# Kernel optimization log

Hardware: AMD Instinct MI355X
Metric: run time of the kernel (lower is better)

## Reference

```python
import jax, jax.numpy as jnp
import numpy as np

EPS = 1e-8  # torch F.cosine_similarity norm clamp


def setup_inputs() -> dict:
    key = jax.random.key(0)
    kq, km = jax.random.split(key)
    b, c, h, w = 4, 128, 16, 16
    n_mem = 2000
    query_feature = jax.random.normal(kq, (b, c, h, w), dtype=jnp.float32)
    memory_bank = jax.random.normal(km, (n_mem, b, c, h, w), dtype=jnp.float32)
    return {"query_feature": query_feature, "memory_bank": memory_bank, "k": 20}


def reference(query_feature, memory_bank, k):
    b = query_feature.shape[0]
    n = memory_bank.shape[0]
    # Flatten per-batch features: query [b, D], memory [N, b, D]
    qf = query_feature.reshape(b, -1)
    mf = memory_bank.reshape(n, b, -1)
    # Cosine similarity along feature dim (torch clamps each norm by eps)
    qn = qf / jnp.maximum(jnp.linalg.norm(qf, axis=-1, keepdims=True), EPS)
    mn = mf / jnp.maximum(jnp.linalg.norm(mf, axis=-1, keepdims=True), EPS)
    sims = jnp.einsum('bd,nbd->n', qn, mn) / b  # mean over batch -> [N]
    top_vals, top_idx = jax.lax.top_k(sims, k)
    weights = jax.nn.softmax(top_vals)  # [k]
    # Weighted gather-sum of selected memory items -> [b, c, h, w]
    selected = memory_bank[top_idx]  # [k, b, c, h, w]
    weighted_sum = jnp.einsum('k,kbchw->bchw', weights, selected)
    return weighted_sum
```

## Files before the change

kernel.cpp:

```cpp
#include <hip/hip_runtime.h>
#include <hip/hip_bf16.h>
#include <math.h>

#define BQ    4
#define DIM   32768
#define DIM4  8192
#define ITEM4 32768
#define EPS   1e-8f
#define QREG  16

__global__ __launch_bounds__(512) void dot_norm_kernel(
        const float* __restrict__ q, const float* __restrict__ mem,
        float2* __restrict__ dn, int N) {
    const int b    = blockIdx.x & 3;
    const int bn   = blockIdx.x >> 2;
    const int nblk = gridDim.x >> 2;
    const int wid  = threadIdx.x >> 6;
    const int lane = threadIdx.x & 63;

    const float4* q4 = (const float4*)(q + (size_t)b * DIM);
    float4 qr[QREG];
    #pragma unroll
    for (int j = 0; j < QREG; ++j) qr[j] = q4[threadIdx.x + j * 512];

    __shared__ float sd[2][8], sn[2][8];
    int buf = 0;

    for (int n = bn; n < N; n += nblk, buf ^= 1) {
        const float4* m4 = (const float4*)(mem + ((size_t)n * BQ + b) * DIM);
        float dot = 0.f, nrm = 0.f;
        #pragma unroll
        for (int j = 0; j < QREG; ++j) {
            float4 m = m4[threadIdx.x + j * 512];
            float4 a = qr[j];
            dot += a.x * m.x + a.y * m.y + a.z * m.z + a.w * m.w;
            nrm += m.x * m.x + m.y * m.y + m.z * m.z + m.w * m.w;
        }
        #pragma unroll
        for (int off = 32; off > 0; off >>= 1) {
            dot += __shfl_down(dot, off);
            nrm += __shfl_down(nrm, off);
        }
        if (lane == 0) { sd[buf][wid] = dot; sn[buf][wid] = nrm; }
        __syncthreads();
        if (threadIdx.x == 0) {
            float d = 0.f, n2 = 0.f;
            #pragma unroll
            for (int w = 0; w < 8; ++w) { d += sd[buf][w]; n2 += sn[buf][w]; }
            dn[n * BQ + b] = make_float2(d, n2);
        }
    }
}

__global__ __launch_bounds__(512) void topk_softmax_kernel(
        const float* __restrict__ q,
        const float2* __restrict__ dn,
        const int* __restrict__ kp,
        float* __restrict__ weights,
        int* __restrict__ topidx,
        int N) {
    const int k    = *kp;
    const int lane = threadIdx.x & 63;
    const int wid  = threadIdx.x >> 6;

    __shared__ float sq[8];
    __shared__ float qden[BQ];
    __shared__ float swv[8];
    __shared__ int   swi[8];
    __shared__ int   sbi;
    __shared__ float tvals[64];
    __shared__ int   tidxs[64];

    {
        const int b = wid & 3, half = wid >> 2;
        const float4* q4 = (const float4*)(q + (size_t)b * DIM) + half * (DIM4 / 2);
        float s = 0.f;
        #pragma unroll 8
        for (int j = 0; j < 64; ++j) {
            float4 v = q4[lane + j * 64];
            s += v.x * v.x + v.y * v.y + v.z * v.z + v.w * v.w;
        }
        #pragma unroll
        for (int off = 32; off > 0; off >>= 1) s += __shfl_down(s, off);
        if (lane == 0) sq[wid] = s;
    }
    __syncthreads();
    if (threadIdx.x < BQ)
        qden[threadIdx.x] = fmaxf(sqrtf(sq[threadIdx.x] + sq[threadIdx.x + 4]), EPS);
    __syncthreads();

    float sv[4];
    #pragma unroll
    for (int i = 0; i < 4; ++i) {
        const int n = threadIdx.x + i * 512;
        if (n < N) {
            const float4* p4 = (const float4*)(dn + (size_t)n * BQ);
            float4 v0 = p4[0];
            float4 v1 = p4[1];
            float s = v0.x / (qden[0] * fmaxf(sqrtf(v0.y), EPS))
                    + v0.z / (qden[1] * fmaxf(sqrtf(v0.w), EPS))
                    + v1.x / (qden[2] * fmaxf(sqrtf(v1.y), EPS))
                    + v1.z / (qden[3] * fmaxf(sqrtf(v1.w), EPS));
            sv[i] = s * (1.0f / BQ);
        } else {
            sv[i] = -INFINITY;
        }
    }

    for (int it = 0; it < k; ++it) {
        float best = sv[0];
        int bi = threadIdx.x;
        #pragma unroll
        for (int i = 1; i < 4; ++i) {
            if (sv[i] > best) { best = sv[i]; bi = threadIdx.x + i * 512; }
        }
        #pragma unroll
        for (int off = 32; off > 0; off >>= 1) {
            float ov = __shfl_down(best, off);
            int   oi = __shfl_down(bi, off);
            if (ov > best || (ov == best && oi < bi)) { best = ov; bi = oi; }
        }
        if (lane == 0) { swv[wid] = best; swi[wid] = bi; }
        __syncthreads();
        if (threadIdx.x == 0) {
            float bv = swv[0]; int bx = swi[0];
            #pragma unroll
            for (int w = 1; w < 8; ++w) {
                if (swv[w] > bv || (swv[w] == bv && swi[w] < bx)) { bv = swv[w]; bx = swi[w]; }
            }
            tvals[it] = bv;
            tidxs[it] = bx;
            sbi = bx;
        }
        __syncthreads();
        const int won = sbi;
        if ((won & 511) == (int)threadIdx.x) sv[won >> 9] = -INFINITY;
    }

    if (threadIdx.x == 0) {
        float m = tvals[0];
        float sum = 0.f;
        for (int i = 0; i < k; ++i) sum += expf(tvals[i] - m);
        float inv = 1.0f / sum;
        for (int i = 0; i < k; ++i) {
            weights[i] = expf(tvals[i] - m) * inv;
            topidx[i]  = tidxs[i];
        }
    }
}

__global__ __launch_bounds__(256) void wsum_kernel(
        const float* __restrict__ mem,
        const float* __restrict__ weights,
        const int* __restrict__ topidx,
        const int* __restrict__ kp,
        float* __restrict__ out) {
    const int k = *kp;
    __shared__ float w[64];
    __shared__ int   id[64];
    if ((int)threadIdx.x < k) {
        w[threadIdx.x]  = weights[threadIdx.x];
        id[threadIdx.x] = topidx[threadIdx.x];
    }
    __syncthreads();
    const int t = blockIdx.x * blockDim.x + threadIdx.x;
    if (t >= ITEM4) return;
    const float4* m4 = (const float4*)mem;
    float4 acc = {0.f, 0.f, 0.f, 0.f};
    for (int j = 0; j < k; ++j) {
        float4 v = m4[(size_t)id[j] * ITEM4 + t];
        float wj = w[j];
        acc.x += wj * v.x; acc.y += wj * v.y; acc.z += wj * v.z; acc.w += wj * v.w;
    }
    ((float4*)out)[t] = acc;
}

extern "C" void kernel_launch(void* const* d_in, const int* in_sizes, int n_in,
                              void* d_out, int out_size, void* d_ws, size_t ws_size,
                              hipStream_t stream) {
    const float* q   = (const float*)d_in[0];
    const float* mem = (const float*)d_in[1];
    const int*   kp  = (const int*)d_in[2];
    float* out = (float*)d_out;

    const int N = in_sizes[1] / (BQ * DIM);

    float2* dn   = (float2*)d_ws;
    float*  wts  = (float*)(dn + (size_t)N * BQ);
    int*    tidx = (int*)(wts + 64);

    dot_norm_kernel<<<2048, 512, 0, stream>>>(q, mem, dn, N);
    topk_softmax_kernel<<<1, 512, 0, stream>>>(q, dn, kp, wts, tidx, N);
    wsum_kernel<<<(ITEM4 + 255) / 256, 256, 0, stream>>>(mem, wts, tidx, kp, out);
}
```

Measured before the change: 217.2 us.

## Use nontemporal streaming loads, single-barrier top-k, and smaller wsum blocks

The memory bank scan in dot_norm now uses nontemporal vector loads so streamed data does not pollute the cache. The top-k loop uses double-buffered shared slots, letting every thread reduce the wave winners itself and dropping one barrier per iteration. The weighted-sum kernel drops to 128-thread blocks and unrolls its gather loop to put more loads in flight. The nontemporal hint may also evict lines that the later gather could have reused.

```diff
diff --git a/kernel.cpp b/kernel.cpp
--- a/kernel.cpp
+++ b/kernel.cpp
@@ -9,6 +9,8 @@
 #define EPS   1e-8f
 #define QREG  16
 
+using f4 = __attribute__((ext_vector_type(4))) float;
+
 __global__ __launch_bounds__(512) void dot_norm_kernel(
         const float* __restrict__ q, const float* __restrict__ mem,
         float2* __restrict__ dn, int N) {
@@ -18,8 +20,8 @@
     const int wid  = threadIdx.x >> 6;
     const int lane = threadIdx.x & 63;
 
-    const float4* q4 = (const float4*)(q + (size_t)b * DIM);
-    float4 qr[QREG];
+    const f4* q4 = (const f4*)(q + (size_t)b * DIM);
+    f4 qr[QREG];
     #pragma unroll
     for (int j = 0; j < QREG; ++j) qr[j] = q4[threadIdx.x + j * 512];
 
@@ -27,12 +29,12 @@
     int buf = 0;
 
     for (int n = bn; n < N; n += nblk, buf ^= 1) {
-        const float4* m4 = (const float4*)(mem + ((size_t)n * BQ + b) * DIM);
+        const f4* m4 = (const f4*)(mem + ((size_t)n * BQ + b) * DIM);
         float dot = 0.f, nrm = 0.f;
         #pragma unroll
         for (int j = 0; j < QREG; ++j) {
-            float4 m = m4[threadIdx.x + j * 512];
-            float4 a = qr[j];
+            f4 m = __builtin_nontemporal_load(m4 + threadIdx.x + j * 512);
+            f4 a = qr[j];
             dot += a.x * m.x + a.y * m.y + a.z * m.z + a.w * m.w;
             nrm += m.x * m.x + m.y * m.y + m.z * m.z + m.w * m.w;
         }
@@ -65,19 +67,18 @@
 
     __shared__ float sq[8];
     __shared__ float qden[BQ];
-    __shared__ float swv[8];
-    __shared__ int   swi[8];
-    __shared__ int   sbi;
+    __shared__ float swv[2][8];
+    __shared__ int   swi[2][8];
     __shared__ float tvals[64];
     __shared__ int   tidxs[64];
 
     {
         const int b = wid & 3, half = wid >> 2;
-        const float4* q4 = (const float4*)(q + (size_t)b * DIM) + half * (DIM4 / 2);
+        const f4* q4 = (const f4*)(q + (size_t)b * DIM) + half * (DIM4 / 2);
         float s = 0.f;
         #pragma unroll 8
         for (int j = 0; j < 64; ++j) {
-            float4 v = q4[lane + j * 64];
+            f4 v = q4[lane + j * 64];
             s += v.x * v.x + v.y * v.y + v.z * v.z + v.w * v.w;
         }
         #pragma unroll
@@ -94,9 +95,9 @@
     for (int i = 0; i < 4; ++i) {
         const int n = threadIdx.x + i * 512;
         if (n < N) {
-            const float4* p4 = (const float4*)(dn + (size_t)n * BQ);
-            float4 v0 = p4[0];
-            float4 v1 = p4[1];
+            const f4* p4 = (const f4*)(dn + (size_t)n * BQ);
+            f4 v0 = p4[0];
+            f4 v1 = p4[1];
             float s = v0.x / (qden[0] * fmaxf(sqrtf(v0.y), EPS))
                     + v0.z / (qden[1] * fmaxf(sqrtf(v0.w), EPS))
                     + v1.x / (qden[2] * fmaxf(sqrtf(v1.y), EPS))
@@ -108,6 +109,7 @@
     }
 
     for (int it = 0; it < k; ++it) {
+        const int par = it & 1;
         float best = sv[0];
         int bi = threadIdx.x;
         #pragma unroll
@@ -120,21 +122,17 @@
             int   oi = __shfl_down(bi, off);
             if (ov > best || (ov == best && oi < bi)) { best = ov; bi = oi; }
         }
-        if (lane == 0) { swv[wid] = best; swi[wid] = bi; }
+        if (lane == 0) { swv[par][wid] = best; swi[par][wid] = bi; }
         __syncthreads();
-        if (threadIdx.x == 0) {
-            float bv = swv[0]; int bx = swi[0];
-            #pragma unroll
-            for (int w = 1; w < 8; ++w) {
-                if (swv[w] > bv || (swv[w] == bv && swi[w] < bx)) { bv = swv[w]; bx = swi[w]; }
+        float bv = swv[par][0]; int bx = swi[par][0];
+        #pragma unroll
+        for (int w = 1; w < 8; ++w) {
+            if (swv[par][w] > bv || (swv[par][w] == bv && swi[par][w] < bx)) {
+                bv = swv[par][w]; bx = swi[par][w];
             }
-            tvals[it] = bv;
-            tidxs[it] = bx;
-            sbi = bx;
         }
-        __syncthreads();
-        const int won = sbi;
-        if ((won & 511) == (int)threadIdx.x) sv[won >> 9] = -INFINITY;
+        if (threadIdx.x == 0) { tvals[it] = bv; tidxs[it] = bx; }
+        if ((bx & 511) == (int)threadIdx.x) sv[bx >> 9] = -INFINITY;
     }
 
     if (threadIdx.x == 0) {
@@ -149,7 +147,7 @@
     }
 }
 
-__global__ __launch_bounds__(256) void wsum_kernel(
+__global__ __launch_bounds__(128) void wsum_kernel(
         const float* __restrict__ mem,
         const float* __restrict__ weights,
         const int* __restrict__ topidx,
@@ -165,14 +163,15 @@
     __syncthreads();
     const int t = blockIdx.x * blockDim.x + threadIdx.x;
     if (t >= ITEM4) return;
-    const float4* m4 = (const float4*)mem;
-    float4 acc = {0.f, 0.f, 0.f, 0.f};
+    const f4* m4 = (const f4*)mem;
+    f4 acc = {0.f, 0.f, 0.f, 0.f};
+    #pragma unroll 4
     for (int j = 0; j < k; ++j) {
-        float4 v = m4[(size_t)id[j] * ITEM4 + t];
+        f4 v = m4[(size_t)id[j] * ITEM4 + t];
         float wj = w[j];
         acc.x += wj * v.x; acc.y += wj * v.y; acc.z += wj * v.z; acc.w += wj * v.w;
     }
-    ((float4*)out)[t] = acc;
+    ((f4*)out)[t] = acc;
 }
 
 extern "C" void kernel_launch(void* const* d_in, const int* in_sizes, int n_in,
@@ -191,5 +190,5 @@
 
     dot_norm_kernel<<<2048, 512, 0, stream>>>(q, mem, dn, N);
     topk_softmax_kernel<<<1, 512, 0, stream>>>(q, dn, kp, wts, tidx, N);
-    wsum_kernel<<<(ITEM4 + 255) / 256, 256, 0, stream>>>(mem, wts, tidx, kp, out);
+    wsum_kernel<<<(ITEM4 + 127) / 128, 128, 0, stream>>>(mem, wts, tidx, kp, out);
 }
```

Result: faster. 191.9 us (-11.7%).
